# Kernel optimization log

Hardware: AMD Instinct MI355X
Metric: run time of the kernel (lower is better)

## Reference

```python
import jax, jax.numpy as jnp
import numpy as np

NUM_CELLS = 2
N = 4096          # num_nodes == layer_1_in (required by the module's shapes)
D1 = 64           # layer_1_out
D2 = 32           # layer_2_out
NH = 4            # n_heads
ALPHA = 0.2       # leaky relu slope


def _xavier(key, shape):
    fan_in, fan_out = shape[-2], shape[-1]
    s = jnp.sqrt(6.0 / (fan_in + fan_out)).astype(jnp.float32)
    return jax.random.uniform(key, shape, jnp.float32, -s, s)


def setup_inputs() -> dict:
    key = jax.random.key(0)
    ks = jax.random.split(key, 9)
    x = jax.random.uniform(ks[0], (NUM_CELLS, N, N), jnp.float32)
    # normalized adjacency (row-stochastic-ish) to keep softmax(adj @ e) sane
    adj = jax.random.uniform(ks[1], (NUM_CELLS, N, N), jnp.float32) / N
    w_init = _xavier(ks[2], (N, D1))                      # weight_l1_init [layer_1_in, layer_1_out]
    head_H = _xavier(ks[3], (NUM_CELLS, NH, D1, D1))      # per-head GAT weight
    head_a = _xavier(ks[4], (NUM_CELLS, NH, 2 * D1, 1))   # per-head attention vector
    out_H = _xavier(ks[5], (NUM_CELLS, NH * D1, D1))      # out_att_l1 weight
    out_a = _xavier(ks[6], (NUM_CELLS, 2 * D1, 1))        # out_att_l1 attention vector
    l2_w = _xavier(ks[7], (NUM_CELLS, D1, D2))            # l2_weight
    return {"x": x, "adj": adj, "w_init": w_init, "head_H": head_H,
            "head_a": head_a, "out_H": out_H, "out_a": out_a, "l2_w": l2_w}


def _gat(xin, adj_c, Hm, av, concat):
    # Faithful to GraphAttentionLayer, but the O(N^2) repeat/cat pairwise build is
    # replaced by the equivalent decomposition e[i,j] = (h_i @ a1) + (h_j @ a2).
    h = xin @ Hm                                  # [N, d]
    d = Hm.shape[1]
    f1 = h @ av[:d]                               # [N, 1]
    f2 = h @ av[d:]                               # [N, 1]
    e = jax.nn.leaky_relu(f1 + f2.T, ALPHA)       # [N, N]
    att = jax.nn.softmax(adj_c @ e, axis=1)       # spmm then row softmax
    hp = att @ h                                  # [N, d]
    return jax.nn.elu(hp) if concat else hp


def reference(x, adj, w_init, head_H, head_a, out_H, out_a, l2_w):
    prev = w_init                                 # layer_1_weights
    h2 = None
    for i in range(NUM_CELLS):
        adj_i = adj[i]
        heads = jax.vmap(lambda Hm, av: _gat(prev, adj_i, Hm, av, True))(head_H[i], head_a[i])  # [NH, N, D1]
        cat = jnp.transpose(heads, (1, 0, 2)).reshape(N, NH * D1)    # concat along features
        x1 = jax.nn.elu(_gat(cat, adj_i, out_H[i], out_a[i], False)) # [N, D1]
        h1 = jax.nn.relu(adj_i @ (x[i] @ x1))                        # [N, D1]
        h2 = adj_i @ (h1 @ l2_w[i])                                  # [N, D2]
        prev = x1
    return h2
```

## Files before the change

kernel.cpp:

```cpp
#include <hip/hip_runtime.h>
#include <hip/hip_bf16.h>
#include <cstdint>
#include <cstddef>

constexpr int Nn = 4096;
constexpr int NB = 64;
constexpr int MC = 3 * NB;

typedef __attribute__((ext_vector_type(8))) short bf16x8;
typedef __attribute__((ext_vector_type(8))) short short8;
typedef __attribute__((ext_vector_type(4))) float f32x4;

__device__ __forceinline__ unsigned short f2bf(float x) {
  union { float f; unsigned u; } v; v.f = x;
  unsigned r = v.u + 0x7FFFu + ((v.u >> 16) & 1u);
  return (unsigned short)(r >> 16);
}
__device__ __forceinline__ float bf2f(unsigned short b) {
  union { unsigned u; float f; } v; v.u = ((unsigned)b) << 16; return v.f;
}

__global__ __launch_bounds__(256) void k_cvt(
    const float* __restrict__ in, unsigned short* __restrict__ out) {
  size_t id = ((size_t)blockIdx.x * 256 + threadIdx.x) * 8;
  const float4 a = *(const float4*)(in + id);
  const float4 b = *(const float4*)(in + id + 4);
  short8 v;
  v[0] = (short)f2bf(a.x); v[1] = (short)f2bf(a.y);
  v[2] = (short)f2bf(a.z); v[3] = (short)f2bf(a.w);
  v[4] = (short)f2bf(b.x); v[5] = (short)f2bf(b.y);
  v[6] = (short)f2bf(b.z); v[7] = (short)f2bf(b.w);
  *(short8*)(out + id) = v;
}

__global__ __launch_bounds__(256) void k_hf4(
    const float* __restrict__ prev, int din,
    const float* __restrict__ Wb, size_t wstride,
    const float* __restrict__ avb, size_t avstride,
    unsigned short* __restrict__ htrb,
    float* __restrict__ f1b, float* __restrict__ f2b) {
  __shared__ float Wl[64 * 64];
  int h = blockIdx.y;
  const float* W  = Wb + (size_t)h * wstride;
  const float* av = avb + (size_t)h * avstride;
  unsigned short* htr = htrb + (size_t)h * 64 * Nn;
  int t = threadIdx.x;
  int r = __builtin_amdgcn_readfirstlane(blockIdx.x * 4 + (t >> 6));
  int d = t & 63;
  const float* pr = prev + (size_t)r * din;
  float acc = 0.f;
  for (int kb = 0; kb < din; kb += 64) {
    for (int i = t; i < 64 * 64; i += 256) Wl[i] = W[kb * 64 + i];
    __syncthreads();
    #pragma unroll 8
    for (int k = 0; k < 64; ++k) acc = fmaf(pr[kb + k], Wl[k * 64 + d], acc);
    __syncthreads();
  }
  htr[(size_t)d * Nn + r] = f2bf(acc);
  float p1 = acc * av[d];
  float p2 = acc * av[64 + d];
  #pragma unroll
  for (int off = 32; off; off >>= 1) {
    p1 += __shfl_down(p1, off);
    p2 += __shfl_down(p2, off);
  }
  if (d == 0) { f1b[h * Nn + r] = p1; f2b[h * Nn + r] = p2; }
}

__global__ __launch_bounds__(256) void k_mbuild(
    const float* __restrict__ f1b, const float* __restrict__ f2b,
    unsigned short* __restrict__ Mb, unsigned char* __restrict__ jbb) {
  __shared__ float fl[Nn];
  __shared__ float red[16];
  int h = blockIdx.y, col = blockIdx.x;
  const float* f1 = f1b + (size_t)h * Nn;
  int t = threadIdx.x, lane = t & 63, wv = t >> 6;
  float lmin = 3e38f, lmax = -3e38f;
  #pragma unroll
  for (int i = 0; i < 16; ++i) {
    float v = f1[i * 256 + t];
    fl[i * 256 + t] = v;
    lmin = fminf(lmin, v); lmax = fmaxf(lmax, v);
  }
  #pragma unroll
  for (int off = 32; off; off >>= 1) {
    lmin = fminf(lmin, __shfl_xor(lmin, off));
    lmax = fmaxf(lmax, __shfl_xor(lmax, off));
  }
  if (lane == 0) { red[wv] = lmin; red[8 + wv] = lmax; }
  __syncthreads();
  float emin = fminf(fminf(red[0], red[1]), fminf(red[2], red[3]));
  float emax = fmaxf(fmaxf(red[8], red[9]), fmaxf(red[10], red[11]));
  float wr = emax - emin;
  float invw = (wr > 0.f) ? (float)NB / wr : 0.f;
  int part = col >> 6, bb = col & 63;
  unsigned short* mrow = Mb + ((size_t)h * MC + col) * Nn;
  #pragma unroll
  for (int i = 0; i < 16; ++i) {
    int k = i * 256 + t;
    float f = fl[k];
    int b = (int)floorf((emax - f) * invw);
    b = b < 0 ? 0 : (b > NB - 1 ? NB - 1 : b);
    unsigned short val = 0;
    if (b == bb) {
      if (part == 0) val = 0x3F80;
      else {
        unsigned short hb = f2bf(f);
        val = (part == 1) ? hb : f2bf(f - bf2f(hb));
      }
    }
    mrow[k] = val;
  }
  if (col == 0) {
    const float* f2 = f2b + (size_t)h * Nn;
    #pragma unroll
    for (int i = 0; i < 16; ++i) {
      int j = i * 256 + t;
      int b = (int)floorf((emax + f2[j]) * invw + 0.5f);
      b = b < 0 ? 0 : (b > NB ? NB : b);
      jbb[(size_t)h * Nn + j] = (unsigned char)b;
    }
  }
}

template<int AMODE, int NCB, bool BSPLIT>
__global__ __launch_bounds__(256) void k_gemm(
    const void* __restrict__ Ap, size_t astride,
    const unsigned short* __restrict__ Bthb,
    const unsigned short* __restrict__ Btlb, size_t bstride,
    float* __restrict__ Cpartb, size_t cstride, int ldc, int CG) {
  constexpr int APL = (AMODE == 2) ? 2 : 1;
  constexpr int BPL = BSPLIT ? 2 : 1;
  constexpr int NT = NCB / 16;
  __shared__ __align__(16) unsigned short Abuf[APL][128][72];
  __shared__ __align__(16) unsigned short Bbuf[BPL][NCB][72];
  int h = blockIdx.z;
  int cg = blockIdx.y % CG;
  int kc = blockIdx.y / CG;
  int SK = gridDim.y / CG;
  int kslice = Nn / SK;
  const unsigned short* Bth = Bthb + (size_t)h * bstride + (size_t)(cg * NCB) * Nn;
  const unsigned short* Btl = BSPLIT
      ? (Btlb + (size_t)h * bstride + (size_t)(cg * NCB) * Nn) : nullptr;
  float* Cpart = Cpartb + (size_t)h * cstride + (size_t)kc * Nn * ldc + cg * NCB;
  int t = threadIdx.x;
  int wv = t >> 6, l = t & 63;
  int l15 = l & 15, lq = l >> 4;
  int row0 = blockIdx.x * 128;
  f32x4 acc[2][NT] = {};
  for (int kt = kc * kslice; kt < (kc + 1) * kslice; kt += 64) {
    __syncthreads();
    #pragma unroll
    for (int i = 0; i < 4; ++i) {
      int cid = i * 256 + t;
      int row = cid >> 3, ch = cid & 7;
      if constexpr (AMODE == 0) {
        bf16x8 v = *(const bf16x8*)((const unsigned short*)Ap +
                     (size_t)h * astride + (size_t)(row0 + row) * Nn + kt + ch * 8);
        *(bf16x8*)&Abuf[0][row][ch * 8] = v;
      } else {
        const float* fp = (const float*)Ap + (size_t)(row0 + row) * Nn + kt + ch * 8;
        const float4 xa = *(const float4*)fp;
        const float4 xb = *(const float4*)(fp + 4);
        float xs[8] = {xa.x, xa.y, xa.z, xa.w, xb.x, xb.y, xb.z, xb.w};
        bf16x8 hi, lo;
        #pragma unroll
        for (int e = 0; e < 8; ++e) {
          unsigned short hb = f2bf(xs[e]);
          hi[e] = (short)hb;
          lo[e] = (short)f2bf(xs[e] - bf2f(hb));
        }
        *(bf16x8*)&Abuf[0][row][ch * 8] = hi;
        *(bf16x8*)&Abuf[APL - 1][row][ch * 8] = lo;
      }
    }
    #pragma unroll
    for (int i = 0; i < NCB / 32; ++i) {
      int cid = i * 256 + t;
      int row = cid >> 3, ch = cid & 7;
      bf16x8 v = *(const bf16x8*)(Bth + (size_t)row * Nn + kt + ch * 8);
      *(bf16x8*)&Bbuf[0][row][ch * 8] = v;
      if constexpr (BSPLIT) {
        bf16x8 w = *(const bf16x8*)(Btl + (size_t)row * Nn + kt + ch * 8);
        *(bf16x8*)&Bbuf[BPL - 1][row][ch * 8] = w;
      }
    }
    __syncthreads();
    #pragma unroll
    for (int k0 = 0; k0 < 64; k0 += 32) {
      bf16x8 a0 = *(const bf16x8*)&Abuf[0][wv * 32 + l15][k0 + lq * 8];
      bf16x8 a1 = *(const bf16x8*)&Abuf[0][wv * 32 + 16 + l15][k0 + lq * 8];
      bf16x8 a0l, a1l;
      if constexpr (AMODE == 2) {
        a0l = *(const bf16x8*)&Abuf[APL - 1][wv * 32 + l15][k0 + lq * 8];
        a1l = *(const bf16x8*)&Abuf[APL - 1][wv * 32 + 16 + l15][k0 + lq * 8];
      }
      #pragma unroll
      for (int ct = 0; ct < NT; ++ct) {
        bf16x8 bh = *(const bf16x8*)&Bbuf[0][ct * 16 + l15][k0 + lq * 8];
        acc[0][ct] = __builtin_amdgcn_mfma_f32_16x16x32_bf16(a0, bh, acc[0][ct], 0, 0, 0);
        acc[1][ct] = __builtin_amdgcn_mfma_f32_16x16x32_bf16(a1, bh, acc[1][ct], 0, 0, 0);
        if constexpr (BSPLIT) {
          bf16x8 bl = *(const bf16x8*)&Bbuf[BPL - 1][ct * 16 + l15][k0 + lq * 8];
          acc[0][ct] = __builtin_amdgcn_mfma_f32_16x16x32_bf16(a0, bl, acc[0][ct], 0, 0, 0);
          acc[1][ct] = __builtin_amdgcn_mfma_f32_16x16x32_bf16(a1, bl, acc[1][ct], 0, 0, 0);
        }
        if constexpr (AMODE == 2) {
          acc[0][ct] = __builtin_amdgcn_mfma_f32_16x16x32_bf16(a0l, bh, acc[0][ct], 0, 0, 0);
          acc[1][ct] = __builtin_amdgcn_mfma_f32_16x16x32_bf16(a1l, bh, acc[1][ct], 0, 0, 0);
        }
      }
    }
  }
  #pragma unroll
  for (int mi = 0; mi < 2; ++mi) {
    #pragma unroll
    for (int ct = 0; ct < NT; ++ct) {
      #pragma unroll
      for (int q = 0; q < 4; ++q) {
        int r = row0 + wv * 32 + mi * 16 + lq * 4 + q;
        Cpart[(size_t)r * ldc + ct * 16 + l15] = acc[mi][ct][q];
      }
    }
  }
}

template<int SK>
__global__ __launch_bounds__(256) void k_sm(
    const float* __restrict__ Hb, const float* __restrict__ f2b,
    const unsigned char* __restrict__ jbb, unsigned short* __restrict__ attb,
    int nh) {
  __shared__ float hr[MC];
  __shared__ float C0x[NB + 1], C1x[NB + 1];
  __shared__ float red[8];
  int t = threadIdx.x;
  int lane = t & 63, wv = t >> 6;
  int r = blockIdx.x;
  for (int h = 0; h < nh; ++h) {
    if (h) __syncthreads();
    if (t < MC) {
      const float* p = Hb + (size_t)h * SK * Nn * MC + (size_t)r * MC + t;
      float s = 0.f;
      #pragma unroll
      for (int sk = 0; sk < SK; ++sk) s += p[(size_t)sk * Nn * MC];
      hr[t] = s;
    }
    __syncthreads();
    if (t < 64) {
      float v0 = hr[t];
      float v1 = hr[64 + t] + hr[128 + t];
      #pragma unroll
      for (int off = 1; off < 64; off <<= 1) {
        float u0 = __shfl_up(v0, off);
        float u1 = __shfl_up(v1, off);
        if (lane >= off) { v0 += u0; v1 += u1; }
      }
      C0x[t + 1] = v0; C1x[t + 1] = v1;
      if (t == 0) { C0x[0] = 0.f; C1x[0] = 0.f; }
    }
    __syncthreads();
    float S0 = C0x[NB], S1 = C1x[NB];
    const float* f2 = f2b + (size_t)h * Nn;
    const unsigned char* jb = jbb + (size_t)h * Nn;
    float sv[16];
    float mx = -3.0e38f;
    #pragma unroll
    for (int c = 0; c < 16; ++c) {
      int j = c * 256 + t;
      float fj = f2[j];
      int b = jb[j];
      float s = 0.2f * fmaf(fj, S0, S1) + 0.8f * fmaf(fj, C0x[b], C1x[b]);
      sv[c] = s;
      mx = fmaxf(mx, s);
    }
    #pragma unroll
    for (int off = 32; off; off >>= 1) mx = fmaxf(mx, __shfl_xor(mx, off));
    __syncthreads();
    if (lane == 0) red[wv] = mx;
    __syncthreads();
    mx = fmaxf(fmaxf(red[0], red[1]), fmaxf(red[2], red[3]));
    float pv[16];
    float sum = 0.f;
    #pragma unroll
    for (int c = 0; c < 16; ++c) { float p = __expf(sv[c] - mx); pv[c] = p; sum += p; }
    #pragma unroll
    for (int off = 32; off; off >>= 1) sum += __shfl_xor(sum, off);
    __syncthreads();
    if (lane == 0) red[4 + wv] = sum;
    __syncthreads();
    float inv = 1.f / (red[4] + red[5] + red[6] + red[7]);
    unsigned short* orow = attb + (size_t)h * Nn * Nn + (size_t)r * Nn;
    #pragma unroll
    for (int c = 0; c < 16; ++c) orow[c * 256 + t] = f2bf(pv[c] * inv);
  }
}

template<int NC, int SK>
__global__ __launch_bounds__(256) void k_red4(
    const float* __restrict__ Cpartb, size_t cph,
    float* __restrict__ dst, int ldd, int coff0, int coffstep, int epi,
    unsigned short* __restrict__ oh, unsigned short* __restrict__ ol) {
  int h = blockIdx.y;
  const float* cp = Cpartb + (size_t)h * cph;
  int id = blockIdx.x * 256 + threadIdx.x;
  int r = id / NC, c = id % NC;
  float s = 0.f;
  #pragma unroll
  for (int kc = 0; kc < SK; ++kc) s += cp[((size_t)kc * Nn + r) * NC + c];
  if (epi == 1) s = (s > 0.f) ? s : expm1f(s);
  else if (epi == 2) s = fmaxf(s, 0.f);
  if (dst) dst[(size_t)r * ldd + coff0 + h * coffstep + c] = s;
  if (oh) {
    unsigned short hb = f2bf(s);
    oh[(size_t)c * Nn + r] = hb;
    if (ol) ol[(size_t)c * Nn + r] = f2bf(s - bf2f(hb));
  }
}

__global__ __launch_bounds__(256) void k_redU(
    const float* __restrict__ Cpart, const float* __restrict__ W,
    unsigned short* __restrict__ ut) {
  __shared__ float hl[4][64];
  __shared__ float Wl[64 * 32];
  int t = threadIdx.x;
  for (int i = t; i < 64 * 32; i += 256) Wl[i] = W[i];
  int id = blockIdx.x * 256 + t;
  int r = id >> 6, c = id & 63;
  float s = 0.f;
  #pragma unroll
  for (int kc = 0; kc < 32; ++kc) s += Cpart[((size_t)kc * Nn + r) * 64 + c];
  hl[t >> 6][c] = fmaxf(s, 0.f);
  __syncthreads();
  if (t < 128) {
    int lr = t >> 5, d = t & 31;
    int row = blockIdx.x * 4 + lr;
    const float* hrr = hl[lr];
    float acc = 0.f;
    #pragma unroll 8
    for (int k = 0; k < 64; ++k) acc = fmaf(hrr[k], Wl[k * 32 + d], acc);
    ut[(size_t)d * Nn + row] = f2bf(acc);
  }
}

extern "C" void kernel_launch(void* const* d_in, const int* in_sizes, int n_in,
                              void* d_out, int out_size, void* d_ws, size_t ws_size,
                              hipStream_t stream) {
  (void)in_sizes; (void)n_in; (void)out_size; (void)ws_size;
  const float* x    = (const float*)d_in[0];
  const float* adj  = (const float*)d_in[1];
  const float* wini = (const float*)d_in[2];
  const float* hH   = (const float*)d_in[3];
  const float* ha   = (const float*)d_in[4];
  const float* oH   = (const float*)d_in[5];
  const float* oa   = (const float*)d_in[6];
  const float* l2w  = (const float*)d_in[7];

  char* ws = (char*)d_ws;
  size_t off = 0;
  auto alloc = [&](size_t bytes) -> void* {
    void* p = ws + off;
    off += (bytes + 4095) & ~(size_t)4095;
    return p;
  };
  unsigned short* adjbf = (unsigned short*)alloc((size_t)Nn * Nn * 2);
  unsigned short* htr4  = (unsigned short*)alloc((size_t)4 * 64 * Nn * 2);
  float* f14            = (float*)alloc((size_t)4 * Nn * 4);
  float* f24            = (float*)alloc((size_t)4 * Nn * 4);
  unsigned char* jb4    = (unsigned char*)alloc((size_t)4 * Nn);
  unsigned short* Mbuf  = (unsigned short*)alloc((size_t)4 * MC * Nn * 2);
  float* Hbuf           = (float*)alloc((size_t)8 * Nn * MC * 4 * 4);
  unsigned short* att4  = (unsigned short*)alloc((size_t)4 * Nn * Nn * 2);
  float* cpart          = (float*)alloc((size_t)32 * Nn * 64 * 4);
  float* cat            = (float*)alloc((size_t)Nn * 256 * 4);
  float* x1             = (float*)alloc((size_t)Nn * 64 * 4);
  unsigned short* bth   = (unsigned short*)alloc((size_t)Nn * 64 * 2);
  unsigned short* btl   = (unsigned short*)alloc((size_t)Nn * 64 * 2);

  const size_t AS  = (size_t)Nn * Nn;
  const size_t BS  = (size_t)64 * Nn;
  const size_t MS  = (size_t)MC * Nn;
  const size_t HS4 = (size_t)4 * Nn * MC;
  const size_t CS8 = (size_t)8 * Nn * 64;

  auto run_stage = [&](const float* xin, int din, const float* Hm, size_t hms,
                       const float* av, size_t avs, int nh) {
    k_hf4<<<dim3(Nn / 4, nh), 256, 0, stream>>>(xin, din, Hm, hms, av, avs,
                                                htr4, f14, f24);
    k_mbuild<<<dim3(MC, nh), 256, 0, stream>>>(f14, f24, Mbuf, jb4);
    if (nh == 4) {
      k_gemm<0, 64, false><<<dim3(32, 12, 4), 256, 0, stream>>>(
          adjbf, 0, Mbuf, nullptr, MS, Hbuf, HS4, MC, 3);
      k_sm<4><<<dim3(Nn), 256, 0, stream>>>(Hbuf, f24, jb4, att4, 4);
      k_gemm<0, 64, false><<<dim3(32, 8, 4), 256, 0, stream>>>(
          att4, AS, htr4, nullptr, BS, cpart, CS8, 64, 1);
    } else {
      k_gemm<0, 64, false><<<dim3(32, 24, 1), 256, 0, stream>>>(
          adjbf, 0, Mbuf, nullptr, MS, Hbuf, 0, MC, 3);
      k_sm<8><<<dim3(Nn), 256, 0, stream>>>(Hbuf, f24, jb4, att4, 1);
      k_gemm<0, 64, false><<<dim3(32, 32, 1), 256, 0, stream>>>(
          att4, 0, htr4, nullptr, 0, cpart, 0, 64, 1);
    }
  };

  const float* prev = wini;
  for (int cell = 0; cell < 2; ++cell) {
    const float* adj_c = adj + (size_t)cell * Nn * Nn;
    k_cvt<<<dim3(Nn * Nn / 8 / 256), 256, 0, stream>>>(adj_c, adjbf);
    run_stage(prev, 64, hH + (size_t)cell * 4 * 64 * 64, (size_t)64 * 64,
              ha + (size_t)cell * 4 * 128, 128, 4);
    k_red4<64, 8><<<dim3(Nn * 64 / 256, 4), 256, 0, stream>>>(
        cpart, CS8, cat, 256, 0, 64, 1, nullptr, nullptr);
    run_stage(cat, 256, oH + (size_t)cell * 256 * 64, 0,
              oa + (size_t)cell * 128, 0, 1);
    if (cell == 0)
      k_red4<64, 32><<<dim3(Nn * 64 / 256, 1), 256, 0, stream>>>(
          cpart, 0, x1, 64, 0, 0, 1, nullptr, nullptr);
    else
      k_red4<64, 32><<<dim3(Nn * 64 / 256, 1), 256, 0, stream>>>(
          cpart, 0, nullptr, 0, 0, 0, 1, bth, btl);
    prev = x1;
  }

  const float* x1c = x + (size_t)Nn * Nn;
  k_gemm<2, 64, true><<<dim3(32, 32, 1), 256, 0, stream>>>(
      x1c, 0, bth, btl, 0, cpart, 0, 64, 1);
  k_red4<64, 32><<<dim3(Nn * 64 / 256, 1), 256, 0, stream>>>(
      cpart, 0, nullptr, 0, 0, 0, 0, bth, nullptr);
  k_gemm<0, 64, false><<<dim3(32, 32, 1), 256, 0, stream>>>(
      adjbf, 0, bth, nullptr, 0, cpart, 0, 64, 1);
  k_redU<<<dim3(Nn / 4), 256, 0, stream>>>(
      cpart, l2w + 64 * 32, bth);
  k_gemm<0, 32, false><<<dim3(32, 32, 1), 256, 0, stream>>>(
      adjbf, 0, bth, nullptr, 0, cpart, 0, 32, 1);
  k_red4<32, 32><<<dim3(Nn * 32 / 256, 1), 256, 0, stream>>>(
      cpart, 0, (float*)d_out, 32, 0, 0, 0, nullptr, nullptr);
}
```

Before: 762.1 us.

## Fuse attention softmax into PV GEMM via per-row score tables, drop N^2 att buffer

The softmax kernel no longer writes a full bf16 N×N attention matrix. It now stores a small per-row table (C0/C1 coefficients plus the log-sum-exp), and a new k_pv kernel recomputes the exp scores on the fly from f2 and the bucket indices, feeding them straight into MFMA against h. This removes the 4×N×N bf16 write and read traffic per stage. The adj×M GEMM is also retiled to wider N (192 and 96) with less K splitting, and the split-K reduction counts are changed to match. The cost is extra exp work inside the GEMM inner loop.

```diff
diff --git a/kernel.cpp b/kernel.cpp
--- a/kernel.cpp
+++ b/kernel.cpp
@@ -6,6 +6,7 @@
 constexpr int Nn = 4096;
 constexpr int NB = 64;
 constexpr int MC = 3 * NB;
+constexpr int TW = 132;
 
 typedef __attribute__((ext_vector_type(8))) short bf16x8;
 typedef __attribute__((ext_vector_type(8))) short short8;
@@ -226,10 +227,10 @@
 }
 
 template<int SK>
-__global__ __launch_bounds__(256) void k_sm(
+__global__ __launch_bounds__(256) void k_tab(
     const float* __restrict__ Hb, const float* __restrict__ f2b,
-    const unsigned char* __restrict__ jbb, unsigned short* __restrict__ attb,
-    int nh) {
+    const unsigned char* __restrict__ jbb, float* __restrict__ tabs,
+    size_t tstride, int nh) {
   __shared__ float hr[MC];
   __shared__ float C0x[NB + 1], C1x[NB + 1];
   __shared__ float red[8];
@@ -279,19 +280,74 @@
     if (lane == 0) red[wv] = mx;
     __syncthreads();
     mx = fmaxf(fmaxf(red[0], red[1]), fmaxf(red[2], red[3]));
-    float pv[16];
     float sum = 0.f;
     #pragma unroll
-    for (int c = 0; c < 16; ++c) { float p = __expf(sv[c] - mx); pv[c] = p; sum += p; }
+    for (int c = 0; c < 16; ++c) sum += __expf(sv[c] - mx);
     #pragma unroll
     for (int off = 32; off; off >>= 1) sum += __shfl_xor(sum, off);
     __syncthreads();
     if (lane == 0) red[4 + wv] = sum;
     __syncthreads();
-    float inv = 1.f / (red[4] + red[5] + red[6] + red[7]);
-    unsigned short* orow = attb + (size_t)h * Nn * Nn + (size_t)r * Nn;
-    #pragma unroll
-    for (int c = 0; c < 16; ++c) orow[c * 256 + t] = f2bf(pv[c] * inv);
+    float mxp = mx + __logf(red[4] + red[5] + red[6] + red[7]);
+    float* tr = tabs + (size_t)h * tstride + (size_t)r * TW;
+    if (t < 65) tr[t] = C0x[t];
+    else if (t < 130) tr[t] = C1x[t - 65];
+    else if (t == 130) tr[130] = mxp;
+  }
+}
+
+template<int DN>
+__global__ __launch_bounds__(256) void k_pv(
+    const float* __restrict__ tabs, size_t tstride,
+    const float* __restrict__ f2b, const unsigned char* __restrict__ jbb,
+    const unsigned short* __restrict__ htrb, size_t bstride,
+    float* __restrict__ cpartb, size_t cstride) {
+  __shared__ float Tf[64 * TW];
+  int h = blockIdx.z;
+  int kc = blockIdx.y;
+  int kslice = Nn / gridDim.y;
+  int row0 = blockIdx.x * 64;
+  const float* tab = tabs + (size_t)h * tstride + (size_t)row0 * TW;
+  int t = threadIdx.x;
+  for (int i = t; i < 64 * TW / 4; i += 256)
+    ((float4*)Tf)[i] = ((const float4*)tab)[i];
+  __syncthreads();
+  int wv = t >> 6, l = t & 63, l15 = l & 15, lq = l >> 4;
+  const float* Tr = Tf + (wv * 16 + l15) * TW;
+  float S0 = Tr[64], S1 = Tr[129], mxp = Tr[130];
+  const float* f2 = f2b + (size_t)h * Nn;
+  const unsigned char* jb = jbb + (size_t)h * Nn;
+  const unsigned short* htr = htrb + (size_t)h * bstride;
+  f32x4 acc[DN / 16] = {};
+  for (int jt = kc * kslice; jt < (kc + 1) * kslice; jt += 32) {
+    int j0 = jt + lq * 8;
+    const float4 fa = *(const float4*)(f2 + j0);
+    const float4 fb = *(const float4*)(f2 + j0 + 4);
+    const uint2 jraw = *(const uint2*)(jb + j0);
+    float fjs[8] = {fa.x, fa.y, fa.z, fa.w, fb.x, fb.y, fb.z, fb.w};
+    bf16x8 af;
+    #pragma unroll
+    for (int e = 0; e < 8; ++e) {
+      unsigned bword = (e < 4) ? jraw.x : jraw.y;
+      int b = (bword >> (8 * (e & 3))) & 255;
+      float fj = fjs[e];
+      float s = 0.2f * fmaf(fj, S0, S1) + 0.8f * fmaf(fj, Tr[b], Tr[65 + b]);
+      af[e] = (short)f2bf(__expf(s - mxp));
+    }
+    #pragma unroll
+    for (int ct = 0; ct < DN / 16; ++ct) {
+      bf16x8 bh = *(const bf16x8*)(htr + (size_t)(ct * 16 + l15) * Nn + j0);
+      acc[ct] = __builtin_amdgcn_mfma_f32_16x16x32_bf16(af, bh, acc[ct], 0, 0, 0);
+    }
+  }
+  float* Cpart = cpartb + (size_t)h * cstride + (size_t)kc * Nn * DN;
+  #pragma unroll
+  for (int ct = 0; ct < DN / 16; ++ct) {
+    #pragma unroll
+    for (int q = 0; q < 4; ++q) {
+      int r = row0 + wv * 16 + lq * 4 + q;
+      Cpart[(size_t)r * DN + ct * 16 + l15] = acc[ct][q];
+    }
   }
 }
 
@@ -368,18 +424,18 @@
   float* f24            = (float*)alloc((size_t)4 * Nn * 4);
   unsigned char* jb4    = (unsigned char*)alloc((size_t)4 * Nn);
   unsigned short* Mbuf  = (unsigned short*)alloc((size_t)4 * MC * Nn * 2);
-  float* Hbuf           = (float*)alloc((size_t)8 * Nn * MC * 4 * 4);
-  unsigned short* att4  = (unsigned short*)alloc((size_t)4 * Nn * Nn * 2);
+  float* Hbuf           = (float*)alloc((size_t)4 * 4 * Nn * MC * 4);
+  float* tabs           = (float*)alloc((size_t)4 * Nn * TW * 4);
   float* cpart          = (float*)alloc((size_t)32 * Nn * 64 * 4);
   float* cat            = (float*)alloc((size_t)Nn * 256 * 4);
   float* x1             = (float*)alloc((size_t)Nn * 64 * 4);
   unsigned short* bth   = (unsigned short*)alloc((size_t)Nn * 64 * 2);
   unsigned short* btl   = (unsigned short*)alloc((size_t)Nn * 64 * 2);
 
-  const size_t AS  = (size_t)Nn * Nn;
   const size_t BS  = (size_t)64 * Nn;
   const size_t MS  = (size_t)MC * Nn;
   const size_t HS4 = (size_t)4 * Nn * MC;
+  const size_t TS  = (size_t)Nn * TW;
   const size_t CS8 = (size_t)8 * Nn * 64;
 
   auto run_stage = [&](const float* xin, int din, const float* Hm, size_t hms,
@@ -388,17 +444,19 @@
                                                 htr4, f14, f24);
     k_mbuild<<<dim3(MC, nh), 256, 0, stream>>>(f14, f24, Mbuf, jb4);
     if (nh == 4) {
-      k_gemm<0, 64, false><<<dim3(32, 12, 4), 256, 0, stream>>>(
-          adjbf, 0, Mbuf, nullptr, MS, Hbuf, HS4, MC, 3);
-      k_sm<4><<<dim3(Nn), 256, 0, stream>>>(Hbuf, f24, jb4, att4, 4);
-      k_gemm<0, 64, false><<<dim3(32, 8, 4), 256, 0, stream>>>(
-          att4, AS, htr4, nullptr, BS, cpart, CS8, 64, 1);
+      k_gemm<0, 192, false><<<dim3(32, 4, 4), 256, 0, stream>>>(
+          adjbf, 0, Mbuf, nullptr, MS, Hbuf, HS4, MC, 1);
+      k_tab<4><<<dim3(Nn), 256, 0, stream>>>(Hbuf, f24, jb4, tabs, TS, 4);
+      k_pv<64><<<dim3(64, 8, 4), 256, 0, stream>>>(
+          tabs, TS, f24, jb4, htr4, BS, cpart, CS8);
+      k_red4<64, 8><<<dim3(Nn * 64 / 256, 4), 256, 0, stream>>>(
+          cpart, CS8, cat, 256, 0, 64, 1, nullptr, nullptr);
     } else {
-      k_gemm<0, 64, false><<<dim3(32, 24, 1), 256, 0, stream>>>(
-          adjbf, 0, Mbuf, nullptr, MS, Hbuf, 0, MC, 3);
-      k_sm<8><<<dim3(Nn), 256, 0, stream>>>(Hbuf, f24, jb4, att4, 1);
-      k_gemm<0, 64, false><<<dim3(32, 32, 1), 256, 0, stream>>>(
-          att4, 0, htr4, nullptr, 0, cpart, 0, 64, 1);
+      k_gemm<0, 96, false><<<dim3(32, 16, 1), 256, 0, stream>>>(
+          adjbf, 0, Mbuf, nullptr, 0, Hbuf, 0, MC, 2);
+      k_tab<8><<<dim3(Nn), 256, 0, stream>>>(Hbuf, f24, jb4, tabs, TS, 1);
+      k_pv<64><<<dim3(64, 16, 1), 256, 0, stream>>>(
+          tabs, TS, f24, jb4, htr4, 0, cpart, 0);
     }
   };
 
@@ -408,15 +466,13 @@
     k_cvt<<<dim3(Nn * Nn / 8 / 256), 256, 0, stream>>>(adj_c, adjbf);
     run_stage(prev, 64, hH + (size_t)cell * 4 * 64 * 64, (size_t)64 * 64,
               ha + (size_t)cell * 4 * 128, 128, 4);
-    k_red4<64, 8><<<dim3(Nn * 64 / 256, 4), 256, 0, stream>>>(
-        cpart, CS8, cat, 256, 0, 64, 1, nullptr, nullptr);
     run_stage(cat, 256, oH + (size_t)cell * 256 * 64, 0,
               oa + (size_t)cell * 128, 0, 1);
     if (cell == 0)
-      k_red4<64, 32><<<dim3(Nn * 64 / 256, 1), 256, 0, stream>>>(
+      k_red4<64, 16><<<dim3(Nn * 64 / 256, 1), 256, 0, stream>>>(
           cpart, 0, x1, 64, 0, 0, 1, nullptr, nullptr);
     else
-      k_red4<64, 32><<<dim3(Nn * 64 / 256, 1), 256, 0, stream>>>(
+      k_red4<64, 16><<<dim3(Nn * 64 / 256, 1), 256, 0, stream>>>(
           cpart, 0, nullptr, 0, 0, 0, 1, bth, btl);
     prev = x1;
   }
```

Result: slower. 912.0 us (+19.7%).
